# Performance work log

Measured on AMD Instinct MI355X. Metric: run time of the kernel, lower is better.

## Reference

```python
import jax, jax.numpy as jnp
import numpy as np

V = 50000      # tokenizer vocab size
E = 128        # embedding_dim
H = 160        # encoder_hidden_dim (bidirectional -> 2H)
D = 196        # decoder_hidden_dim
A = 224        # attention_dim
BN = 56        # bottle_neck_dim
PAD, START, END, UNK = 0, 1, 2, 3
COV_FACTOR = 0.75


def _lstm_step(x, h, c, Wi, Wh, bi, bh):
    # torch gate order: i, f, g, o
    g = x @ Wi.T + h @ Wh.T + bi + bh
    i, f, gg, o = jnp.split(g, 4, axis=-1)
    c = jax.nn.sigmoid(f) * c + jax.nn.sigmoid(i) * jnp.tanh(gg)
    h = jax.nn.sigmoid(o) * jnp.tanh(c)
    return h, c


def _run_lstm(x_tbe, Wi, Wh, bi, bh):
    B = x_tbe.shape[1]
    Hh = Wh.shape[1]
    def step(carry, xt):
        h, c = carry
        h, c = _lstm_step(xt, h, c, Wi, Wh, bi, bh)
        return (h, c), h
    init = (jnp.zeros((B, Hh), x_tbe.dtype), jnp.zeros((B, Hh), x_tbe.dtype))
    (hT, cT), hs = jax.lax.scan(step, init, x_tbe)
    return hs, hT, cT


def setup_inputs() -> dict:
    key = jax.random.key(0)
    ks = iter(jax.random.split(key, 48))
    def rn(shape, s=0.05):
        return jax.random.normal(next(ks), shape, jnp.float32) * s
    B, Tin, Ttgt = 32, 256, 100
    inp = {
        'batch_input_ids': jax.random.randint(next(ks), (B, Tin), 0, V + 50, dtype=jnp.int32),
        'batch_target_ids': jax.random.randint(next(ks), (B, Ttgt), 0, V + 50, dtype=jnp.int32),
        'max_num_oovs': 50,
        'emb': rn((V, E), 0.1),
        # bidirectional encoder LSTM
        'Wi_f': rn((4 * H, E)), 'Wh_f': rn((4 * H, H)),
        'bi_f': jnp.zeros(4 * H), 'bh_f': jnp.zeros(4 * H),
        'Wi_b': rn((4 * H, E)), 'Wh_b': rn((4 * H, H)),
        'bi_b': jnp.zeros(4 * H), 'bh_b': jnp.zeros(4 * H),
        # enc->dec bridges
        'Weh': rn((D, 2 * H)), 'beh': jnp.zeros(D),
        'Wec': rn((D, 2 * H)), 'bec': jnp.zeros(D),
        # decoder LSTMCell
        'Wi_d': rn((4 * D, E)), 'Wh_d': rn((4 * D, D)),
        'bi_d': jnp.zeros(4 * D), 'bh_d': jnp.zeros(4 * D),
        # attention
        'Wea': rn((A, 2 * H)), 'bea': jnp.zeros(A),
        'Wda': rn((A, D)),
        'Wca': rn((A, 1)),
        'v_attn': rn((1, A)),
        # vocab projection (bottleneck)
        'W1': rn((BN, D + 2 * H)), 'b1': jnp.zeros(BN),
        'W2': rn((V - END, BN)), 'b2': jnp.zeros(V - END),
        # p_gen switch
        'Wcs': rn((1, 2 * H)), 'bcs': jnp.zeros(1),
        'Wds': rn((1, D)),
        'Wes': rn((1, E)),
    }
    return inp


def reference(batch_input_ids, batch_target_ids, max_num_oovs, emb,
              Wi_f, Wh_f, bi_f, bh_f, Wi_b, Wh_b, bi_b, bh_b,
              Weh, beh, Wec, bec, Wi_d, Wh_d, bi_d, bh_d,
              Wea, bea, Wda, Wca, v_attn, W1, b1, W2, b2,
              Wcs, bcs, Wds, Wes):
    B, Tin = batch_input_ids.shape
    # map OOV input ids to <unk> for embedding lookup
    in_mapped = jnp.where(batch_input_ids >= V, UNK, batch_input_ids)
    x_tbe = emb[in_mapped].transpose(1, 0, 2)          # [Tin,B,E]
    hs_f, hTf, cTf = _run_lstm(x_tbe, Wi_f, Wh_f, bi_f, bh_f)
    hs_b, hTb, cTb = _run_lstm(x_tbe[::-1], Wi_b, Wh_b, bi_b, bh_b)
    enc = jnp.concatenate([hs_f, hs_b[::-1]], -1).transpose(1, 0, 2)  # [B,Tin,2H]
    h = jnp.concatenate([hTf, hTb], -1) @ Weh.T + beh   # [B,D]
    c = jnp.concatenate([cTf, cTb], -1) @ Wec.T + bec   # [B,D]
    enc_attn = enc @ Wea.T + bea                        # [B,Tin,A] (loop-invariant)
    pad_mask = batch_input_ids == PAD
    wca = Wca[:, 0]                                     # [A]
    cov0 = jnp.zeros((B, Tin))
    cur0 = jnp.full((B,), START, jnp.int32)

    def step(carry, nt):
        h, c, cov, cur, nll, cl = carry
        e = emb[cur]                                     # [B,E]
        h, c = _lstm_step(e, h, c, Wi_d, Wh_d, bi_d, bh_d)
        s = jnp.tanh(enc_attn + (h @ Wda.T)[:, None, :] + cov[:, :, None] * wca)
        s = s @ v_attn[0]                                # [B,Tin]
        s = jnp.where(pad_mask, -jnp.inf, s)
        attn = jax.nn.softmax(s, axis=1)                 # [B,Tin]
        ctx = jnp.einsum('bt,bth->bh', attn, enc)        # [B,2H]
        hc = jnp.concatenate([h, ctx], -1)
        vocab = jax.nn.softmax(jnp.tanh(hc @ W1.T + b1) @ W2.T + b2, axis=1)  # [B,V-END]
        p_gen = jax.nn.sigmoid(ctx @ Wcs[0] + bcs[0] + h @ Wds[0] + e @ Wes[0])  # [B]
        # F.pad(vocab, (END, max_num_oovs)).gather(1, nt): left-pad END zeros,
        # right-pad OOV zeros -> gen prob is vocab[nt-END] if END<=nt<V else 0
        idx = jnp.clip(nt - END, 0, vocab.shape[1] - 1)
        gen_p = jnp.take_along_axis(vocab, idx[:, None], axis=1)[:, 0]
        gen_p = jnp.where((nt >= END) & (nt < V), gen_p, 0.0)
        copy_p = jnp.sum(attn * (batch_input_ids == nt[:, None]), axis=1)
        p = p_gen * gen_p + (1.0 - p_gen) * copy_p
        nll = nll - jnp.log(p + 1e-9)
        cl = cl + jnp.minimum(attn, cov).sum(axis=1)
        cov = cov + attn
        cur = jnp.where(nt >= V, UNK, nt)
        return (h, c, cov, cur, nll, cl), None

    (h, c, cov, cur, nll, cl), _ = jax.lax.scan(
        step, (h, c, cov0, cur0, jnp.zeros(B), jnp.zeros(B)), batch_target_ids.T)
    nll_loss = nll.sum()
    cov_loss = cl.sum()
    return nll_loss, cov_loss, nll_loss + COV_FACTOR * cov_loss
```

## Files before the change

### kernel.cpp

```cpp
#include <hip/hip_runtime.h>

#define MSCOPE __HIP_MEMORY_SCOPE_AGENT


constexpr size_t oXf   = 0;
constexpr size_t oXb   = oXf   + (size_t)8192*640;
constexpr size_t oXd   = oXb   + (size_t)8192*640;
constexpr size_t oHencB= oXd   + (size_t)3200*784;
constexpr size_t oEncA = oHencB+ (size_t)64*256*160;
constexpr size_t oEs   = oEncA + (size_t)8192*224;
constexpr size_t oCT   = oEs   + 3200;
constexpr size_t oH0   = oCT   + 10240;
constexpr size_t oC0   = oH0   + 6272;
constexpr size_t oHWdsAll = oC0 + 6272;
constexpr size_t oCtxWAll = oHWdsAll + 3200;
constexpr size_t oCopyAll = oCtxWAll + 3200;
constexpr size_t oZidxAll = oCopyAll + 3200;
constexpr size_t oClAll   = oZidxAll + 3200;
constexpr size_t oNllWg   = oClAll + 32;
constexpr size_t oW1cT    = oNllWg + 192;
constexpr size_t oFEnd    = oW1cT + 17920;
constexpr size_t oHdAll   = 0;
constexpr size_t oUAll    = oHdAll + (size_t)100*6272;
constexpr size_t oUPreAll = oUAll  + (size_t)100*1792;
constexpr size_t oHwdaAll = oUPreAll + (size_t)100*1792;
constexpr size_t oPartAll = oHwdaAll + (size_t)100*7168;
#define FENC(d,t,p)  ((((d)*256 + (t))*20 + (p))*16)
#define FLSTM(s,p)   (163840 + ((s)*25 + (p))*16)
#define FAUX(s,p)    (203840 + ((s)*8 + (p))*16)
#define FP2(s,m,p)   (216640 + (((s)*4 + (m))*32 + (p))*16)
#define CP3          421440
#define CFIN         421456
constexpr int fEnd = 421472;

__device__ __forceinline__ float fast_tanh(float x){
  float e = __expf(-2.f*fabsf(x));
  float r = (1.f - e) * __builtin_amdgcn_rcpf(1.f + e);
  return copysignf(r, x);
}
__device__ __forceinline__ float sigm(float x){
  return __builtin_amdgcn_rcpf(1.f + __expf(-x));
}
__device__ __forceinline__ float aload(const float* p){
  return __hip_atomic_load(const_cast<float*>(p), __ATOMIC_RELAXED, MSCOPE);
}
__device__ __forceinline__ float2 aload2(const float* p){
  unsigned long long u = __hip_atomic_load(
      reinterpret_cast<unsigned long long*>(const_cast<float*>(p)),
      __ATOMIC_RELAXED, MSCOPE);
  float2 r; __builtin_memcpy(&r, &u, 8); return r;
}
__device__ __forceinline__ void astore(float* p, float v){
  __hip_atomic_store(p, v, __ATOMIC_RELAXED, MSCOPE);
}
__device__ __forceinline__ void set_line(unsigned* line){
  __hip_atomic_store(line, 1u, __ATOMIC_RELAXED, MSCOPE);
}
template<int SLP>
__device__ __forceinline__ void wait_lines(unsigned* base, int n, int tid){
  if (tid < 64){
    for(;;){
      bool miss = (tid < n) &&
        (__hip_atomic_load(base + tid*16, __ATOMIC_RELAXED, MSCOPE) == 0u);
      if (__ballot(miss) == 0ULL) break;
      __builtin_amdgcn_s_sleep(SLP);
    }
  }
  __syncthreads();
}
__device__ __forceinline__ void add1(unsigned* word){
  (void)__hip_atomic_fetch_add(word, 1u, __ATOMIC_RELAXED, MSCOPE);
}
__device__ __forceinline__ float block_sum(float v, float* red){
  #pragma unroll
  for (int o=32;o;o>>=1) v += __shfl_down(v,o);
  if ((threadIdx.x&63)==0) red[threadIdx.x>>6] = v;
  __syncthreads();
  v = red[0]+red[1]+red[2]+red[3];
  __syncthreads();
  return v;
}

__global__ void prep_kernel(const int* __restrict__ in_ids, const int* __restrict__ tgt,
                            int* __restrict__ in_mapped, int* __restrict__ cur_ids,
                            unsigned* __restrict__ flags){
  const int g0 = blockIdx.x*256 + threadIdx.x, stride = gridDim.x*256;
  for (int i = g0; i < 8192; i += stride){
    int t = i >> 5, b = i & 31;
    int id = in_ids[b*256 + t];
    in_mapped[i] = (id >= 50000) ? 3 : id;
  }
  for (int i = g0; i < 3200; i += stride){
    int k = i >> 5, b = i & 31;
    int id = (k == 0) ? 1 : tgt[b*100 + (k-1)];
    cur_ids[i] = (id >= 50000) ? 3 : id;
  }
  for (int i = g0; i < fEnd; i += stride) flags[i] = 0u;
}

__global__ void w1c_transpose(const float* __restrict__ W1, float* __restrict__ W1cT){
  int i = blockIdx.x*256 + threadIdx.x;
  if (i < 17920){ int q = i / 56, g = i - q*56; W1cT[q*56+g] = W1[(size_t)g*516 + 196 + q]; }
}

struct RGArgs{ const int* gid; const float* emb; const float* W;
               const float* bias1; const float* bias2; float* out; int N; };
__global__ void __launch_bounds__(256) rowgemm(RGArgs a){
  __shared__ float rl[8*128];
  const int tid = threadIdx.x;
  const int N = a.N;
  const size_t r0 = (size_t)blockIdx.x*8;
  const size_t t = r0 >> 5; const int b0 = (int)(r0 & 31);
  for (int i = tid; i < 8*128; i += 256){
    int r = i >> 7, k = i & 127;
    rl[i] = a.emb[(size_t)a.gid[r0+r]*128 + k];
  }
  __syncthreads();
  for (int g = tid; g < N; g += 256){
    const float* wr = a.W + (size_t)g*128;
    float acc[8];
    #pragma unroll
    for (int r=0;r<8;r++) acc[r]=0.f;
    for (int k=0;k<128;k+=4){
      float4 wv = *(const float4*)(wr+k);
      #pragma unroll
      for (int r=0;r<8;r++){
        float4 xv = *(const float4*)(rl + r*128 + k);
        acc[r] += wv.x*xv.x + wv.y*xv.y + wv.z*xv.z + wv.w*xv.w;
      }
    }
    float bias = a.bias1[g] + a.bias2[g];
    float* op = a.out + ((size_t)t*N + g)*32 + b0;
    *(float4*)(op)   = make_float4(acc[0]+bias,acc[1]+bias,acc[2]+bias,acc[3]+bias);
    *(float4*)(op+4) = make_float4(acc[4]+bias,acc[5]+bias,acc[6]+bias,acc[7]+bias);
  }
}

__global__ void es_kernel(const int* __restrict__ gid, const float* __restrict__ emb,
                          const float* __restrict__ Wes, float* __restrict__ es){
  int r = blockIdx.x, l = threadIdx.x;
  const float* e = emb + (size_t)gid[r]*128;
  float acc = e[l]*Wes[l] + e[l+64]*Wes[l+64];
  #pragma unroll
  for (int o=32;o;o>>=1) acc += __shfl_down(acc,o);
  if (l==0) es[r] = acc;
}

struct EncArgs{ const float* Xf; const float* Xb; const float* Whf; const float* Whb;
                float* hencB; float* cT; unsigned* flg; };
__global__ void __launch_bounds__(256) enc_scan(EncArgs a){
  extern __shared__ float sm[];
  float* Wl = sm;
  float* hl = sm + 5120;
  const int wg = blockIdx.x;
  const int dir = wg/20, jwg = wg%20;
// ... 57 lines not shown
  __shared__ float hc[320], cc[320];
  int b = blockIdx.x, tid = threadIdx.x;
  if (tid < 160){
    hc[tid]     = hencB[((size_t)b*256 + 255)*160 + tid];
    hc[160+tid] = hencB[((size_t)(32+b)*256 + 0)*160 + tid];
    cc[tid]     = cT[b*160 + tid];
    cc[160+tid] = cT[5120 + b*160 + tid];
  }
  __syncthreads();
  for (int g = tid; g < 196; g += 256){
    const float* w1 = Weh + (size_t)g*320;
    const float* w2 = Wec + (size_t)g*320;
    float a1 = beh[g], a2 = bec[g];
    for (int k = 0; k < 320; ++k){ a1 += hc[k]*w1[k]; a2 += cc[k]*w2[k]; }
    h0[b*196 + g] = a1;
    c0[b*196 + g] = a2;
  }
}

__global__ void __launch_bounds__(256) encA_gemm(const float* __restrict__ hencB,
                 const float* __restrict__ Wea, const float* __restrict__ bea,
                 float* __restrict__ encA){
  __shared__ float rl[8*320];
  const int tid = threadIdx.x;
  const size_t r0 = (size_t)blockIdx.x*8;
  for (int i = tid; i < 8*320; i += 256){
    int r = i/320, k = i - r*320;
    size_t row = r0 + r; int b = (int)(row >> 8), t = (int)(row & 255);
    rl[i] = (k < 160) ? hencB[((size_t)b*256 + t)*160 + k]
                      : hencB[((size_t)(32+b)*256 + t)*160 + (k-160)];
  }
  __syncthreads();
  for (int g = tid; g < 224; g += 256){
    const float* wr = Wea + (size_t)g*320;
    float acc[8];
    #pragma unroll
    for (int r=0;r<8;r++) acc[r]=0.f;
    for (int k=0;k<320;k+=4){
      float4 wv = *(const float4*)(wr+k);
      #pragma unroll
      for (int r=0;r<8;r++){
        float4 xv = *(const float4*)(rl + r*320 + k);
        acc[r] += wv.x*xv.x + wv.y*xv.y + wv.z*xv.z + wv.w*xv.w;
      }
    }
    float bias = bea[g];
    #pragma unroll
    for (int r=0;r<8;r++) encA[(r0+r)*224 + g] = acc[r] + bias;
  }
}

struct DecArgs{
  const float* Xd; const float* hencB; const float* encA;
  const float* h0; const float* c0;
  const float* Whd; const float* Wda; const float* Wca; const float* vat;
  const float* W1; const float* b1; const float* W1cT; const float* W2; const float* b2;
  const float* Wcs; const float* bcs; const float* Wds; const float* es;
  const int* in_ids; const int* tgt;
  float* hdAll; float* uAll; float* uPreAll; float* hwdaAll;
  float* hWdsAll; float* ctxWAll; float* copyAll;
  float* zidxAll; float* partAll; float* clAll; float* nllWg; float* out;
  unsigned* flg;
};

__device__ __forceinline__ void load_scr(const float* hp, float* scr, int tid){
  for (int i2 = tid; i2 < 3136; i2 += 256){
    float2 hv = aload2(hp + i2*2);
    int e = i2*2; int b2 = e & 31; int j2 = e >> 5;
    scr[b2*204 + j2]     = hv.x;
    scr[(b2+1)*204 + j2] = hv.y;
  }
}

__global__ void __launch_bounds__(256) dec_scan(DecArgs A){
  extern __shared__ float sm[];
  const int wg = blockIdx.x, tid = threadIdx.x;
  const int bp = tid & 31, jl = tid >> 5;
  unsigned* flg = A.flg;

  if (wg < 25){
    const int wl = wg;
    const int j = wl*8 + jl;
    float* Wl  = sm;
    float* scr = sm + 6272;
    for (int i = tid; i < 32*196; i += 256){
      int row = i/196, k = i - row*196;
      int gate = row >> 3, jj = row & 7;
      int jg = wl*8 + jj;
      Wl[i] = (jg < 196) ? A.Whd[((size_t)(gate*196 + jg))*196 + k] : 0.f;
    }
    float c = (j < 196) ? A.c0[bp*196 + j] : 0.f;
    for (int i = tid; i < 6272; i += 256){
      int bb = i/196, k = i - bb*196;
      scr[bb*204 + k] = A.h0[i];
    }
    const float4* w0 = (const float4*)(Wl + (0*8+jl)*196);
    const float4* w1 = (const float4*)(Wl + (1*8+jl)*196);
    const float4* w2 = (const float4*)(Wl + (2*8+jl)*196);
    const float4* w3 = (const float4*)(Wl + (3*8+jl)*196);
    __syncthreads();
    for (int s = 0; s < 100; ++s){
      float x0=0.f,x1=0.f,x2=0.f,x3=0.f;
      if (j < 196){
        const float* xr = A.Xd + ((size_t)s*784 + j)*32 + bp;
        x0 = xr[0]; x1 = xr[6272]; x2 = xr[12544]; x3 = xr[18816];
      }
      if (s > 0){
        wait_lines<2>(flg + FLSTM(s-1, 0), 25, tid);
        load_scr(A.hdAll + (size_t)(s-1)*6272, scr, tid);
      }
      __syncthreads();
      if (j < 196){
        float g0=x0,g1=x1,g2=x2,g3=x3;
        const float4* hr = (const float4*)(scr + bp*204);
        #pragma unroll 7
        for (int q = 0; q < 49; ++q){
          float4 hv = hr[q];
          float4 a0 = w0[q], a1 = w1[q], a2 = w2[q], a3 = w3[q];
          g0 += hv.x*a0.x + hv.y*a0.y + hv.z*a0.z + hv.w*a0.w;
          g1 += hv.x*a1.x + hv.y*a1.y + hv.z*a1.z + hv.w*a1.w;
          g2 += hv.x*a2.x + hv.y*a2.y + hv.z*a2.z + hv.w*a2.w;
          g3 += hv.x*a3.x + hv.y*a3.y + hv.z*a3.z + hv.w*a3.w;
        }
        float ig = sigm(g0), fg = sigm(g1), gc = fast_tanh(g2), og = sigm(g3);
        c = fg*c + ig*gc;
        float h = og * fast_tanh(c);
        astore(&A.hdAll[(size_t)s*6272 + j*32 + bp], h);
      }
      __syncthreads();
      if (tid == 0) set_line(flg + FLSTM(s, wl));
    }
    return;
  }

  if (wg < 33){
    const int a_ = wg - 25;
    float* wdaL = sm;
    float* w1hL = sm + 5488;
    float* WdsL = sm + 6860;
    float* scr  = sm + 7056;
    for (int i = tid; i < 28*196; i += 256){
      int al = i/196, k = i - al*196;
      wdaL[i] = A.Wda[(size_t)(a_*28 + al)*196 + k];
    }
    for (int i = tid; i < 7*196; i += 256){
      int gl = i/196, k = i - gl*196;
      w1hL[i] = A.W1[(size_t)(a_*7 + gl)*516 + k];
    }
    if (a_ == 7) for (int i = tid; i < 196; i += 256) WdsL[i] = A.Wds[i];
    __syncthreads();
    for (int s = 0; s < 100; ++s){
      wait_lines<2>(flg + FLSTM(s, 0), 25, tid);
      load_scr(A.hdAll + (size_t)s*6272, scr, tid);
      __syncthreads();
      for (int i = tid; i < 896; i += 256){
        int b2 = i & 31, al = i >> 5;
        const float4* h4 = (const float4*)(scr + b2*204);
        const float4* w4 = (const float4*)(wdaL + al*196);
        float acc = 0.f;
        #pragma unroll 7
        for (int q = 0; q < 49; ++q){
          float4 a4 = h4[q], b4 = w4[q];
          acc += a4.x*b4.x + a4.y*b4.y + a4.z*b4.z + a4.w*b4.w;
        }
        astore(&A.hwdaAll[(size_t)s*7168 + b2*224 + a_*28 + al], acc);
      }
      if (tid < 224){
        int b2 = tid & 31, gl = tid >> 5;
        int g = a_*7 + gl;
        const float4* h4 = (const float4*)(scr + b2*204);
        const float4* w4 = (const float4*)(w1hL + gl*196);
        float acc = A.b1[g];
        #pragma unroll 7
        for (int q = 0; q < 49; ++q){
          float4 a4 = h4[q], b4 = w4[q];
          acc += a4.x*b4.x + a4.y*b4.y + a4.z*b4.z + a4.w*b4.w;
        }
        astore(&A.uPreAll[(size_t)s*1792 + b2*56 + g], acc);
      }
      if (a_ == 7 && tid < 32){
        const float* hb = scr + tid*204;
        float acc = 0.f;
        #pragma unroll 4
        for (int q = 0; q < 196; ++q) acc += hb[q]*WdsL[q];
        astore(&A.hWdsAll[s*32 + tid], acc);
      }
      __syncthreads();
      if (tid == 0) set_line(flg + FAUX(s, a_));
    }
    return;
  }

  if (wg < 65){
    const int b = wg - 33;
    float* hwdaL = sm;
    float* attnL = sm + 224;
    float* pctx  = sm + 480;
    float* ctxL  = sm + 1440;
    float* red   = sm + 1760;
    float* pu    = sm + 1764;
    float* wcaL  = sm + 1988;
    float* vL    = sm + 2212;
    float* WcsL  = sm + 2436;
    if (tid < 224){ wcaL[tid] = A.Wca[tid]; vL[tid] = A.vat[tid]; }
    for (int i = tid; i < 320; i += 256) WcsL[i] = A.Wcs[i];
    const int inid = A.in_ids[b*256 + tid];
    const float4* erow = (const float4*)(A.encA + (size_t)(b*256 + tid)*224);
    float cov = 0.f, clr = 0.f;
    __syncthreads();
    for (int s = 0; s < 100; ++s){
      wait_lines<2>(flg + FAUX(s, 0), 8, tid);
      if (tid < 224) hwdaL[tid] = aload(&A.hwdaAll[(size_t)s*7168 + b*224 + tid]);
      __syncthreads();
      float exv = 0.f;
      if (inid != 0){
        float acc = 0.f;
        #pragma unroll 8
        for (int q = 0; q < 56; ++q){
          float4 ev = erow[q]; int a0 = 4*q;
          acc += fast_tanh(ev.x + hwdaL[a0]   + cov*wcaL[a0]  )*vL[a0];
          acc += fast_tanh(ev.y + hwdaL[a0+1] + cov*wcaL[a0+1])*vL[a0+1];
          acc += fast_tanh(ev.z + hwdaL[a0+2] + cov*wcaL[a0+2])*vL[a0+2];
          acc += fast_tanh(ev.w + hwdaL[a0+3] + cov*wcaL[a0+3])*vL[a0+3];
        }
        exv = __expf(acc);
      }
      float S = block_sum(exv, red);
      float attn = exv * __builtin_amdgcn_rcpf(S);
      attnL[tid] = attn;
      const int ntb = A.tgt[b*100 + s];
      float cpS = block_sum((inid == ntb) ? attn : 0.f, red);
      float mnS = block_sum(fminf(attn, cov), red);
      if (tid == 0){
        astore(&A.copyAll[s*32 + b], cpS);
        clr += mnS;
        if (s == 99) astore(&A.clAll[b], clr);
      }
      cov += attn;
      if (tid < 240){
        int seg = tid/80, h4i = tid - seg*80;
        int t0 = seg*86, t1 = (t0+86 < 256) ? t0+86 : 256;
        const float* base = (h4i < 40)
          ? (A.hencB + ((size_t)b*256)*160 + (size_t)h4i*4)
          : (A.hencB + ((size_t)(32+b)*256)*160 + (size_t)(h4i-40)*4);
        float4 accv = {0.f,0.f,0.f,0.f};
        #pragma unroll 4
        for (int t2 = t0; t2 < t1; ++t2){
          float av = attnL[t2];
          float4 ev = *(const float4*)(base + (size_t)t2*160);
          accv.x += av*ev.x; accv.y += av*ev.y; accv.z += av*ev.z; accv.w += av*ev.w;
        }
        *(float4*)(pctx + (seg*80+h4i)*4) = accv;
      }
      __syncthreads();
      if (tid < 80){
        float4 p0 = *(float4*)(pctx + tid*4);
        float4 p1 = *(float4*)(pctx + (80+tid)*4);
        float4 p2v = *(float4*)(pctx + (160+tid)*4);
        float4 cvv;
        cvv.x = p0.x+p1.x+p2v.x; cvv.y = p0.y+p1.y+p2v.y;
        cvv.z = p0.z+p1.z+p2v.z; cvv.w = p0.w+p1.w+p2v.w;
        *(float4*)(ctxL + tid*4) = cvv;
      }
      __syncthreads();
      if (tid < 224){
        int g = tid % 56, seg = tid / 56;
        float acc = 0.f;
        const float* wp = A.W1cT + (size_t)seg*80*56 + g;
        #pragma unroll 4
        for (int q = 0; q < 80; ++q) acc += ctxL[seg*80 + q] * wp[q*56];
        pu[seg*56 + g] = acc;
      } else {
        int l = tid - 224; float acc = 0.f;
        for (int q = l; q < 320; q += 32) acc += ctxL[q]*WcsL[q];
        #pragma unroll
        for (int o=16;o;o>>=1) acc += __shfl_down(acc,o,32);
        if (l==0) astore(&A.ctxWAll[s*32 + b], acc);
      }
      __syncthreads();
      if (tid < 56){
        float upre = aload(&A.uPreAll[(size_t)s*1792 + b*56 + tid]);
        float uu = fast_tanh(upre + pu[tid] + pu[56+tid] + pu[112+tid] + pu[168+tid]);
        astore(&A.uAll[(size_t)s*1792 + b*56 + tid], uu);
      }
      __syncthreads();
      if (tid == 0){
        set_line(flg + FP2(s,0,b));
        set_line(flg + FP2(s,1,b));
        set_line(flg + FP2(s,2,b));
        set_line(flg + FP2(s,3,b));
      }
    }
    return;
  }

  {
    const int wgv = wg - 65;
    const int vs = (int)(((long long)wgv*49998)/191);
    const int ve = (int)(((long long)(wgv+1)*49998)/191);
    const int r0v = vs + tid;
    const int r1v = vs + 256 + tid;
    const bool v1 = r1v < ve;
    float4 w2r0[14], w2r1[14];
    {
      const float4* wr = (const float4*)(A.W2 + (size_t)r0v*56);
      #pragma unroll
      for (int q=0;q<14;++q) w2r0[q] = wr[q];
      const float4* wr1 = (const float4*)(A.W2 + (size_t)(v1 ? r1v : vs)*56);
      #pragma unroll
      for (int q=0;q<14;++q) w2r1[q] = wr1[q];
    }
    const float b2v0 = A.b2[r0v];
    const float b2v1 = v1 ? A.b2[r1v] : 0.f;
    float* ulL  = sm;
    float* redW = sm + 1792;
    int*   idxL = (int*)(sm + 1920);
    float* red  = sm + 1952;
    const int lane = tid & 63, wv2 = tid >> 6;
    for (int s = 0; s < 100; ++s){
      int nt3 = (tid < 32) ? A.tgt[tid*100 + s] : 0;
      wait_lines<8>(flg + FP2(s, wgv & 3, 0), 32, tid);
      for (int i2 = tid; i2 < 896; i2 += 256){
        float2 u2 = aload2(&A.uAll[(size_t)s*1792 + i2*2]);
        *(float2*)(ulL + i2*2) = u2;
      }
      if (tid < 32){
        int ix = nt3 - 2; ix = ix<0?0:(ix>49997?49997:ix);
        idxL[tid] = ix;
      }
      __syncthreads();
      #pragma unroll 4
      for (int bb=0; bb<32; ++bb){
        const float4* uv = (const float4*)(ulL + bb*56);
        float z = b2v0;
        #pragma unroll
        for (int q=0;q<14;++q){
          float4 u4 = uv[q];
          z += w2r0[q].x*u4.x + w2r0[q].y*u4.y + w2r0[q].z*u4.z + w2r0[q].w*u4.w;
        }
        if (r0v == idxL[bb]) astore(&A.zidxAll[s*32+bb], z);
        float sv2 = __expf(z);
        if (v1){
          float z1 = b2v1;
          #pragma unroll
          for (int q=0;q<14;++q){
            float4 u4 = uv[q];
            z1 += w2r1[q].x*u4.x + w2r1[q].y*u4.y + w2r1[q].z*u4.z + w2r1[q].w*u4.w;
          }
          if (r1v == idxL[bb]) astore(&A.zidxAll[s*32+bb], z1);
          sv2 += __expf(z1);
        }
        #pragma unroll
        for (int o=32;o;o>>=1) sv2 += __shfl_down(sv2,o);
        if (lane == 0) redW[wv2*32+bb] = sv2;
      }
      __syncthreads();
      if (tid < 32){
        float tot = redW[tid]+redW[32+tid]+redW[64+tid]+redW[96+tid];
        astore(&A.partAll[(size_t)(s*32+tid)*191 + wgv], tot);
      }
      __syncthreads();
    }
    __syncthreads();
    if (tid == 0) add1(flg + CP3);
    if (tid == 0){
      while (__hip_atomic_load(flg + CP3, __ATOMIC_RELAXED, MSCOPE) != 191u)
        __builtin_amdgcn_s_sleep(32);
    }
    __syncthreads();
    float nll1 = 0.f;
    for (int p = wgv; p < 3200; p += 191){
      float pv = (tid < 191) ? aload(&A.partAll[(size_t)p*191 + tid]) : 0.f;
      float se = block_sum(pv, red);
      if (tid == 0){
        int s = p >> 5, b = p & 31;
        int nt2 = A.tgt[b*100 + s];
        float xg = aload(&A.ctxWAll[p]) + A.bcs[0] + aload(&A.hWdsAll[p]) + A.es[p];
        float pg = 1.f/(1.f + __expf(-xg));
        float genp = (nt2 >= 2 && nt2 < 50000) ? (__expf(aload(&A.zidxAll[p])) / se) : 0.f;
        float pr = pg*genp + (1.f-pg)*aload(&A.copyAll[p]);
        nll1 += -logf(pr + 1e-9f);
      }
    }
    if (tid == 0) astore(&A.nllWg[wgv], nll1);
    __syncthreads();
    if (tid == 0) add1(flg + CFIN);
    if (wg == 65){
      if (tid == 0){
        while (__hip_atomic_load(flg + CFIN, __ATOMIC_RELAXED, MSCOPE) != 191u)
          __builtin_amdgcn_s_sleep(32);
      }
      __syncthreads();
      float nv = (tid < 191) ? aload(&A.nllWg[tid]) : 0.f;
      float nll = block_sum(nv, red);
      float cv = (tid < 32) ? aload(&A.clAll[tid]) : 0.f;
      float cl = block_sum(cv, red);
      if (tid == 0){ A.out[0]=nll; A.out[1]=cl; A.out[2]=nll + 0.75f*cl; }
    }
  }
}

extern "C" void kernel_launch(void* const* d_in, const int* in_sizes, int n_in,
                              void* d_out, int out_size, void* d_ws, size_t ws_size,
                              hipStream_t stream){
  const int*   in_ids = (const int*)  d_in[0];
  const int*   tgt    = (const int*)  d_in[1];
  const float* emb    = (const float*)d_in[3];
  const float* Wi_f   = (const float*)d_in[4];
  const float* Wh_f   = (const float*)d_in[5];
  const float* bi_f   = (const float*)d_in[6];
  const float* bh_f   = (const float*)d_in[7];
  const float* Wi_b   = (const float*)d_in[8];
  const float* Wh_b   = (const float*)d_in[9];
  const float* bi_b   = (const float*)d_in[10];
  const float* bh_b   = (const float*)d_in[11];
  const float* Weh    = (const float*)d_in[12];
  const float* beh    = (const float*)d_in[13];
  const float* Wec    = (const float*)d_in[14];
  const float* bec    = (const float*)d_in[15];
  const float* Wi_d   = (const float*)d_in[16];
  const float* Wh_d   = (const float*)d_in[17];
  const float* bi_d   = (const float*)d_in[18];
  const float* bh_d   = (const float*)d_in[19];
  const float* Wea    = (const float*)d_in[20];
  const float* bea    = (const float*)d_in[21];
  const float* Wda    = (const float*)d_in[22];
  const float* Wca    = (const float*)d_in[23];
  const float* vat    = (const float*)d_in[24];
  const float* W1     = (const float*)d_in[25];
  const float* b1     = (const float*)d_in[26];
  const float* W2     = (const float*)d_in[27];
  const float* b2     = (const float*)d_in[28];
  const float* Wcs    = (const float*)d_in[29];
  const float* bcs    = (const float*)d_in[30];
  const float* Wds    = (const float*)d_in[31];
  const float* Wes    = (const float*)d_in[32];

  float* ws = (float*)d_ws;
  int* iBase = (int*)(ws + oFEnd);
  int* in_mapped = iBase;
  int* cur_ids   = iBase + 8192;
  unsigned* flags = (unsigned*)(iBase + 11392);

  prep_kernel<<<512, 256, 0, stream>>>(in_ids, tgt, in_mapped, cur_ids, flags);
  w1c_transpose<<<70, 256, 0, stream>>>(W1, ws + oW1cT);

  { RGArgs a{in_mapped, emb, Wi_f, bi_f, bh_f, ws + oXf, 640};
    rowgemm<<<1024, 256, 0, stream>>>(a); }
  { RGArgs a{in_mapped, emb, Wi_b, bi_b, bh_b, ws + oXb, 640};
    rowgemm<<<1024, 256, 0, stream>>>(a); }
  { RGArgs a{cur_ids, emb, Wi_d, bi_d, bh_d, ws + oXd, 784};
    rowgemm<<<400, 256, 0, stream>>>(a); }

  es_kernel<<<3200, 64, 0, stream>>>(cur_ids, emb, Wes, ws + oEs);

  { EncArgs ea{ws + oXf, ws + oXb, Wh_f, Wh_b, ws + oHencB, ws + oCT, flags};
    void* ka[] = {&ea};
    hipLaunchCooperativeKernel((void*)enc_scan, dim3(40), dim3(256), ka,
                               (unsigned)((5120 + 32*164)*4), stream); }

  mid_kernel<<<32, 256, 0, stream>>>(ws + oHencB, ws + oCT, Weh, beh, Wec, bec,
                                     ws + oH0, ws + oC0);

  encA_gemm<<<1024, 256, 0, stream>>>(ws + oHencB, Wea, bea, ws + oEncA);

  { DecArgs da{ws + oXd, ws + oHencB, ws + oEncA,
               ws + oH0, ws + oC0,
               Wh_d, Wda, Wca, vat,
               W1, b1, ws + oW1cT, W2, b2, Wcs, bcs, Wds, ws + oEs,
               in_ids, tgt,
               ws + oHdAll, ws + oUAll, ws + oUPreAll, ws + oHwdaAll,
               ws + oHWdsAll, ws + oCtxWAll, ws + oCopyAll,
               ws + oZidxAll, ws + oPartAll, ws + oClAll, ws + oNllWg, (float*)d_out,
               flags};
    void* ka[] = {&da};
    hipLaunchCooperativeKernel((void*)dec_scan, dim3(256), dim3(256), ka,
                               (unsigned)(13584*4), stream); }
}
```

Baseline: 4.925 ms.

## Add aggregator workgroup publishing watermark counters for cross-stage step flags

One workgroup (wg 65) is repurposed as a flag aggregator. It polls the per-step LSTM, aux and attention completion lines and publishes monotone watermark counters, replicated over 8 cache lines. Consumers now spin on a single watermark line with one thread instead of ballot-polling 8 to 32 lines each, and the attention stage sets one flag per batch instead of four copies. The intent is to cut polling traffic and contention on the flag lines. The cost is one fewer vocab workgroup (190 instead of 191) and an extra hop of latency through the aggregator.

```diff
diff --git a/kernel.cpp b/kernel.cpp
--- a/kernel.cpp
+++ b/kernel.cpp
@@ -28,10 +28,13 @@
 #define FENC(d,t,p)  ((((d)*256 + (t))*20 + (p))*16)
 #define FLSTM(s,p)   (163840 + ((s)*25 + (p))*16)
 #define FAUX(s,p)    (203840 + ((s)*8 + (p))*16)
-#define FP2(s,m,p)   (216640 + (((s)*4 + (m))*32 + (p))*16)
-#define CP3          421440
-#define CFIN         421456
-constexpr int fEnd = 421472;
+#define FP2(s,b)     (216640 + ((s)*32 + (b))*16)
+#define WML(r)       (267840 + (r)*16)
+#define WMA(r)       (267968 + (r)*16)
+#define WMP(r)       (268096 + (r)*16)
+#define CP3          268224
+#define CFIN         268240
+constexpr int fEnd = 268256;
 
 __device__ __forceinline__ float fast_tanh(float x){
   float e = __expf(-2.f*fabsf(x));
@@ -53,18 +56,30 @@
 __device__ __forceinline__ void astore(float* p, float v){
   __hip_atomic_store(p, v, __ATOMIC_RELAXED, MSCOPE);
 }
+__device__ __forceinline__ unsigned uload(unsigned* p){
+  return __hip_atomic_load(p, __ATOMIC_RELAXED, MSCOPE);
+}
 __device__ __forceinline__ void set_line(unsigned* line){
   __hip_atomic_store(line, 1u, __ATOMIC_RELAXED, MSCOPE);
+}
+__device__ __forceinline__ void ustore(unsigned* line, unsigned v){
+  __hip_atomic_store(line, v, __ATOMIC_RELAXED, MSCOPE);
 }
 template<int SLP>
 __device__ __forceinline__ void wait_lines(unsigned* base, int n, int tid){
   if (tid < 64){
     for(;;){
-      bool miss = (tid < n) &&
-        (__hip_atomic_load(base + tid*16, __ATOMIC_RELAXED, MSCOPE) == 0u);
+      bool miss = (tid < n) && (uload(base + tid*16) == 0u);
       if (__ballot(miss) == 0ULL) break;
       __builtin_amdgcn_s_sleep(SLP);
     }
+  }
+  __syncthreads();
+}
+template<int SLP>
+__device__ __forceinline__ void wait_wm(unsigned* line, unsigned target, int tid){
+  if (tid == 0){
+    while (uload(line) < target) __builtin_amdgcn_s_sleep(SLP);
   }
   __syncthreads();
 }
@@ -362,7 +377,7 @@
     if (a_ == 7) for (int i = tid; i < 196; i += 256) WdsL[i] = A.Wds[i];
     __syncthreads();
     for (int s = 0; s < 100; ++s){
-      wait_lines<2>(flg + FLSTM(s, 0), 25, tid);
+      wait_wm<2>(flg + WML(a_ & 7), (unsigned)(s+1), tid);
       load_scr(A.hdAll + (size_t)s*6272, scr, tid);
       __syncthreads();
       for (int i = tid; i < 896; i += 256){
@@ -421,7 +436,7 @@
     float cov = 0.f, clr = 0.f;
     __syncthreads();
     for (int s = 0; s < 100; ++s){
-      wait_lines<2>(flg + FAUX(s, 0), 8, tid);
+      wait_wm<2>(flg + WMA(b & 7), (unsigned)(s+1), tid);
       if (tid < 224) hwdaL[tid] = aload(&A.hwdaAll[(size_t)s*7168 + b*224 + tid]);
       __syncthreads();
       float exv = 0.f;
@@ -496,20 +511,50 @@
         astore(&A.uAll[(size_t)s*1792 + b*56 + tid], uu);
       }
       __syncthreads();
-      if (tid == 0){
-        set_line(flg + FP2(s,0,b));
-        set_line(flg + FP2(s,1,b));
-        set_line(flg + FP2(s,2,b));
-        set_line(flg + FP2(s,3,b));
-      }
+      if (tid == 0) set_line(flg + FP2(s, b));
     }
     return;
   }
 
+  if (wg == 65){
+    if (tid < 64){
+      int wmL = 0, wmA = 0, wmP = 0;
+      while (wmL < 100 || wmA < 100 || wmP < 100){
+        bool prog = false;
+        if (wmL < 100){
+          bool miss = (tid < 25) && (uload(flg + FLSTM(wmL, tid)) == 0u);
+          if (__ballot(miss) == 0ULL){
+            wmL++;
+            if (tid < 8) ustore(flg + WML(tid), (unsigned)wmL);
+            prog = true;
+          }
+        }
+        if (wmA < 100){
+          bool miss = (tid < 8) && (uload(flg + FAUX(wmA, tid)) == 0u);
+          if (__ballot(miss) == 0ULL){
+            wmA++;
+            if (tid < 8) ustore(flg + WMA(tid), (unsigned)wmA);
+            prog = true;
+          }
+        }
+        if (wmP < 100){
+          bool miss = (tid < 32) && (uload(flg + FP2(wmP, tid)) == 0u);
+          if (__ballot(miss) == 0ULL){
+            wmP++;
+            if (tid < 8) ustore(flg + WMP(tid), (unsigned)wmP);
+            prog = true;
+          }
+        }
+        if (!prog) __builtin_amdgcn_s_sleep(2);
+      }
+    }
+    return;
+  }
+
   {
-    const int wgv = wg - 65;
-    const int vs = (int)(((long long)wgv*49998)/191);
-    const int ve = (int)(((long long)(wgv+1)*49998)/191);
+    const int wgv = wg - 66;
+    const int vs = (int)(((long long)wgv*49998)/190);
+    const int ve = (int)(((long long)(wgv+1)*49998)/190);
     const int r0v = vs + tid;
     const int r1v = vs + 256 + tid;
     const bool v1 = r1v < ve;
@@ -531,7 +576,7 @@
     const int lane = tid & 63, wv2 = tid >> 6;
     for (int s = 0; s < 100; ++s){
       int nt3 = (tid < 32) ? A.tgt[tid*100 + s] : 0;
-      wait_lines<8>(flg + FP2(s, wgv & 3, 0), 32, tid);
+      wait_wm<8>(flg + WMP(wgv & 7), (unsigned)(s+1), tid);
       for (int i2 = tid; i2 < 896; i2 += 256){
         float2 u2 = aload2(&A.uAll[(size_t)s*1792 + i2*2]);
         *(float2*)(ulL + i2*2) = u2;
@@ -569,20 +614,19 @@
       __syncthreads();
       if (tid < 32){
         float tot = redW[tid]+redW[32+tid]+redW[64+tid]+redW[96+tid];
-        astore(&A.partAll[(size_t)(s*32+tid)*191 + wgv], tot);
+        astore(&A.partAll[(size_t)(s*32+tid)*190 + wgv], tot);
       }
       __syncthreads();
     }
     __syncthreads();
     if (tid == 0) add1(flg + CP3);
     if (tid == 0){
-      while (__hip_atomic_load(flg + CP3, __ATOMIC_RELAXED, MSCOPE) != 191u)
-        __builtin_amdgcn_s_sleep(32);
+      while (uload(flg + CP3) != 190u) __builtin_amdgcn_s_sleep(32);
     }
     __syncthreads();
     float nll1 = 0.f;
-    for (int p = wgv; p < 3200; p += 191){
-      float pv = (tid < 191) ? aload(&A.partAll[(size_t)p*191 + tid]) : 0.f;
+    for (int p = wgv; p < 3200; p += 190){
+      float pv = (tid < 190) ? aload(&A.partAll[(size_t)p*190 + tid]) : 0.f;
       float se = block_sum(pv, red);
       if (tid == 0){
         int s = p >> 5, b = p & 31;
@@ -597,13 +641,12 @@
     if (tid == 0) astore(&A.nllWg[wgv], nll1);
     __syncthreads();
     if (tid == 0) add1(flg + CFIN);
-    if (wg == 65){
+    if (wg == 66){
       if (tid == 0){
-        while (__hip_atomic_load(flg + CFIN, __ATOMIC_RELAXED, MSCOPE) != 191u)
-          __builtin_amdgcn_s_sleep(32);
-      }
-      __syncthreads();
-      float nv = (tid < 191) ? aload(&A.nllWg[tid]) : 0.f;
+        while (uload(flg + CFIN) != 190u) __builtin_amdgcn_s_sleep(32);
+      }
+      __syncthreads();
+      float nv = (tid < 190) ? aload(&A.nllWg[tid]) : 0.f;
       float nll = block_sum(nv, red);
       float cv = (tid < 32) ? aload(&A.clAll[tid]) : 0.f;
       float cl = block_sum(cv, red);
```

Result: no change. 4.936 ms (+0.2%).

## Run decoder LSTM recurrence in one workgroup with bf16 MFMA

Applied to the files above, without the earlier changes.

The decoder LSTM recurrence and the hidden-state projections (Wda, W1 hidden part, Wds) are merged into a single workgroup. That workgroup keeps h in LDS as bf16 fragments and computes gates with MFMA 16x16x32 bf16, using weights pre-packed by a new pack_af kernel. This removes the 25-workgroup cross-CU flag handshake and the global hdAll round trip on every step, and frees workgroups so the vocab softmax stage now spans 223 groups of one row per thread. The costs are bf16 rounding of the recurrent weights and state, a serial recurrence on one CU, and a switch from cooperative launch to a normal launch that relies on all workgroups being co-resident for the spin-waits.

```diff
diff --git a/kernel.cpp b/kernel.cpp
--- a/kernel.cpp
+++ b/kernel.cpp
@@ -1,6 +1,9 @@
 #include <hip/hip_runtime.h>
 
 #define MSCOPE __HIP_MEMORY_SCOPE_AGENT
+
+typedef __attribute__((ext_vector_type(8))) short bf16x8;
+typedef __attribute__((ext_vector_type(4))) float f32x4;
 
 
 constexpr size_t oXf   = 0;
@@ -18,20 +21,21 @@
 constexpr size_t oZidxAll = oCopyAll + 3200;
 constexpr size_t oClAll   = oZidxAll + 3200;
 constexpr size_t oNllWg   = oClAll + 32;
-constexpr size_t oW1cT    = oNllWg + 192;
-constexpr size_t oFEnd    = oW1cT + 17920;
-constexpr size_t oHdAll   = 0;
-constexpr size_t oUAll    = oHdAll + (size_t)100*6272;
+constexpr size_t oW1cT    = oNllWg + 224;
+constexpr size_t oAFl     = oW1cT + 17920;
+constexpr size_t oAFa     = oAFl + 93184;
+constexpr size_t oFEnd    = oAFa + 32256;
+constexpr size_t oUAll    = 0;
 constexpr size_t oUPreAll = oUAll  + (size_t)100*1792;
 constexpr size_t oHwdaAll = oUPreAll + (size_t)100*1792;
 constexpr size_t oPartAll = oHwdaAll + (size_t)100*7168;
 #define FENC(d,t,p)  ((((d)*256 + (t))*20 + (p))*16)
-#define FLSTM(s,p)   (163840 + ((s)*25 + (p))*16)
-#define FAUX(s,p)    (203840 + ((s)*8 + (p))*16)
-#define FP2(s,m,p)   (216640 + (((s)*4 + (m))*32 + (p))*16)
-#define CP3          421440
-#define CFIN         421456
-constexpr int fEnd = 421472;
+#define FL(s)        (163840 + (s)*16)
+#define FP2(s,m,b)   (165440 + (((s)*4 + (m))*32 + (b))*16)
+#define CP3          370240
+#define CFIN         370256
+constexpr int fEnd = 370272;
+constexpr unsigned ENC_FULL  = 0xFFFFFu;
 
 __device__ __forceinline__ float fast_tanh(float x){
   float e = __expf(-2.f*fabsf(x));
@@ -40,6 +44,10 @@
 }
 __device__ __forceinline__ float sigm(float x){
   return __builtin_amdgcn_rcpf(1.f + __expf(-x));
+}
+__device__ __forceinline__ unsigned bfr(float f){
+  unsigned u = __float_as_uint(f);
+  return (u + 0x7FFFu + ((u>>16)&1u)) >> 16;
 }
 __device__ __forceinline__ float aload(const float* p){
   return __hip_atomic_load(const_cast<float*>(p), __ATOMIC_RELAXED, MSCOPE);
@@ -53,6 +61,15 @@
 __device__ __forceinline__ void astore(float* p, float v){
   __hip_atomic_store(p, v, __ATOMIC_RELAXED, MSCOPE);
 }
+__device__ __forceinline__ void astore2(float* p, float a, float b){
+  float2 t; t.x = a; t.y = b;
+  unsigned long long u; __builtin_memcpy(&u, &t, 8);
+  __hip_atomic_store(reinterpret_cast<unsigned long long*>(p), u,
+                     __ATOMIC_RELAXED, MSCOPE);
+}
+__device__ __forceinline__ unsigned uload(unsigned* p){
+  return __hip_atomic_load(p, __ATOMIC_RELAXED, MSCOPE);
+}
 __device__ __forceinline__ void set_line(unsigned* line){
   __hip_atomic_store(line, 1u, __ATOMIC_RELAXED, MSCOPE);
 }
@@ -60,8 +77,7 @@
 __device__ __forceinline__ void wait_lines(unsigned* base, int n, int tid){
   if (tid < 64){
     for(;;){
-      bool miss = (tid < n) &&
-        (__hip_atomic_load(base + tid*16, __ATOMIC_RELAXED, MSCOPE) == 0u);
+      bool miss = (tid < n) && (uload(base + tid*16) == 0u);
       if (__ballot(miss) == 0ULL) break;
       __builtin_amdgcn_s_sleep(SLP);
     }
@@ -101,6 +117,48 @@
 __global__ void w1c_transpose(const float* __restrict__ W1, float* __restrict__ W1cT){
   int i = blockIdx.x*256 + threadIdx.x;
   if (i < 17920){ int q = i / 56, g = i - q*56; W1cT[q*56+g] = W1[(size_t)g*516 + 196 + q]; }
+}
+
+__global__ void pack_af(const float* __restrict__ Whd, float* __restrict__ AFl,
+                        const float* __restrict__ Wda, const float* __restrict__ W1,
+                        const float* __restrict__ Wds, float* __restrict__ AFa){
+  int dw = blockIdx.x*256 + threadIdx.x;
+  if (dw < 93184){
+    int frag = dw>>2, d = dw&3;
+    int T = frag/448, r2 = frag - T*448;
+    int k7 = r2>>6, l = r2&63;
+    int jb = T>>2, gate = T&3;
+    int j = jb*16 + (l&15);
+    int k0 = k7*32 + ((l>>4)<<3) + 2*d;
+    unsigned lo=0, hi=0;
+    if (j < 196){
+      if (k0   < 196) lo = bfr(Whd[(size_t)(gate*196+j)*196 + k0]);
+      if (k0+1 < 196) hi = bfr(Whd[(size_t)(gate*196+j)*196 + k0+1]);
+    }
+    ((unsigned*)AFl)[dw] = lo | (hi<<16);
+  }
+  if (dw < 32256){
+    int frag = dw>>2, d = dw&3;
+    int T = frag/448, r2 = frag - T*448;
+    int k7 = r2>>6, l = r2&63;
+    int ar = T*16 + (l&15);
+    int k0 = k7*32 + ((l>>4)<<3) + 2*d;
+    unsigned lo=0, hi=0;
+    #pragma unroll
+    for (int h = 0; h < 2; ++h){
+      int k = k0 + h;
+      float v = 0.f;
+      if (k < 196){
+        if (ar < 224) v = Wda[(size_t)ar*196 + k];
+        else { int g = ar - 224;
+          if (g < 56) v = W1[(size_t)g*516 + k];
+          else if (g == 56) v = Wds[k];
+        }
+      }
+      if (h == 0) lo = bfr(v); else hi = bfr(v);
+    }
+    ((unsigned*)AFa)[dw] = lo | (hi<<16);
+  }
 }
 
 struct RGArgs{ const int* gid; const float* emb; const float* W;
@@ -264,147 +322,163 @@
 
 struct DecArgs{
   const float* Xd; const float* hencB; const float* encA;
-  const float* h0; const float* c0;
-  const float* Whd; const float* Wda; const float* Wca; const float* vat;
-  const float* W1; const float* b1; const float* W1cT; const float* W2; const float* b2;
-  const float* Wcs; const float* bcs; const float* Wds; const float* es;
+  const float* h0; const float* c0; const float* AFl; const float* AFa;
+  const float* Wca; const float* vat; const float* W1cT; const float* b1;
+  const float* W2; const float* b2;
+  const float* Wcs; const float* bcs; const float* es;
   const int* in_ids; const int* tgt;
-  float* hdAll; float* uAll; float* uPreAll; float* hwdaAll;
+  float* uAll; float* uPreAll; float* hwdaAll;
   float* hWdsAll; float* ctxWAll; float* copyAll;
   float* zidxAll; float* partAll; float* clAll; float* nllWg; float* out;
   unsigned* flg;
 };
 
-__device__ __forceinline__ void load_scr(const float* hp, float* scr, int tid){
-  for (int i2 = tid; i2 < 3136; i2 += 256){
-    float2 hv = aload2(hp + i2*2);
-    int e = i2*2; int b2 = e & 31; int j2 = e >> 5;
-    scr[b2*204 + j2]     = hv.x;
-    scr[(b2+1)*204 + j2] = hv.y;
-  }
-}
-
 __global__ void __launch_bounds__(256) dec_scan(DecArgs A){
   extern __shared__ float sm[];
   const int wg = blockIdx.x, tid = threadIdx.x;
-  const int bp = tid & 31, jl = tid >> 5;
   unsigned* flg = A.flg;
 
-  if (wg < 25){
-    const int wl = wg;
-    const int j = wl*8 + jl;
-    float* Wl  = sm;
-    float* scr = sm + 6272;
-    for (int i = tid; i < 32*196; i += 256){
-      int row = i/196, k = i - row*196;
-      int gate = row >> 3, jj = row & 7;
-      int jg = wl*8 + jj;
-      Wl[i] = (jg < 196) ? A.Whd[((size_t)(gate*196 + jg))*196 + k] : 0.f;
-    }
-    float c = (j < 196) ? A.c0[bp*196 + j] : 0.f;
-    for (int i = tid; i < 6272; i += 256){
-      int bb = i/196, k = i - bb*196;
-      scr[bb*204 + k] = A.h0[i];
-    }
-    const float4* w0 = (const float4*)(Wl + (0*8+jl)*196);
-    const float4* w1 = (const float4*)(Wl + (1*8+jl)*196);
-    const float4* w2 = (const float4*)(Wl + (2*8+jl)*196);
-    const float4* w3 = (const float4*)(Wl + (3*8+jl)*196);
+  if (wg == 0){
+    unsigned* bfd = (unsigned*)sm;
+    bf16x8* bfp = (bf16x8*)sm;
+    const bf16x8* afl = (const bf16x8*)A.AFl;
+    const bf16x8* afa = (const bf16x8*)A.AFa;
+    const int l = tid & 63, wv = tid >> 6;
+    const int lq = l >> 4, lc = l & 15;
+    for (int dw = tid; dw < 3584; dw += 256){
+      int frag = dw>>2, d = dw&3;
+      int knt = frag>>6, fl2 = frag&63;
+      int nt = knt&1, k7 = knt>>1;
+      int j0 = k7*32 + ((fl2>>4)<<3) + 2*d;
+      int b = nt*16 + (fl2&15);
+      unsigned lo = (j0   < 196) ? bfr(A.h0[b*196 + j0])   : 0u;
+      unsigned hi = (j0+1 < 196) ? bfr(A.h0[b*196 + j0+1]) : 0u;
+      bfd[dw] = lo | (hi<<16);
+    }
+    float cst[4][2][4];
+    #pragma unroll
+    for (int n = 0; n < 4; ++n){
+      int jb = wv + 4*n;
+      #pragma unroll
+      for (int nt = 0; nt < 2; ++nt){
+        int b = nt*16 + lc;
+        #pragma unroll
+        for (int i = 0; i < 4; ++i){
+          int j = jb*16 + lq*4 + i;
+          cst[n][nt][i] = (jb < 13 && j < 196) ? A.c0[b*196 + j] : 0.f;
+        }
+      }
+    }
     __syncthreads();
+    bf16x8 Bfr[7][2];
+    #pragma unroll
+    for (int k7 = 0; k7 < 7; ++k7)
+      #pragma unroll
+      for (int nt = 0; nt < 2; ++nt)
+        Bfr[k7][nt] = bfp[(k7*2+nt)*64 + l];
+
+    float hreg[4][2][4];
     for (int s = 0; s < 100; ++s){
-      float x0=0.f,x1=0.f,x2=0.f,x3=0.f;
-      if (j < 196){
-        const float* xr = A.Xd + ((size_t)s*784 + j)*32 + bp;
-        x0 = xr[0]; x1 = xr[6272]; x2 = xr[12544]; x3 = xr[18816];
-      }
-      if (s > 0){
-        wait_lines<2>(flg + FLSTM(s-1, 0), 25, tid);
-        load_scr(A.hdAll + (size_t)(s-1)*6272, scr, tid);
-      }
-      __syncthreads();
-      if (j < 196){
-        float g0=x0,g1=x1,g2=x2,g3=x3;
-        const float4* hr = (const float4*)(scr + bp*204);
-        #pragma unroll 7
-        for (int q = 0; q < 49; ++q){
-          float4 hv = hr[q];
-          float4 a0 = w0[q], a1 = w1[q], a2 = w2[q], a3 = w3[q];
-          g0 += hv.x*a0.x + hv.y*a0.y + hv.z*a0.z + hv.w*a0.w;
-          g1 += hv.x*a1.x + hv.y*a1.y + hv.z*a1.z + hv.w*a1.w;
-          g2 += hv.x*a2.x + hv.y*a2.y + hv.z*a2.z + hv.w*a2.w;
-          g3 += hv.x*a3.x + hv.y*a3.y + hv.z*a3.z + hv.w*a3.w;
+      const float* Xs = A.Xd + (size_t)s*25088;
+      #pragma unroll
+      for (int n = 0; n < 4; ++n){
+        int jb = wv + 4*n;
+        if (jb < 13){
+          f32x4 acc[2][4];
+          #pragma unroll
+          for (int g = 0; g < 4; ++g){
+            int T = jb*4 + g;
+            const bf16x8* afT = afl + (size_t)T*7*64 + l;
+            f32x4 a0 = {0.f,0.f,0.f,0.f}, a1 = {0.f,0.f,0.f,0.f};
+            #pragma unroll
+            for (int k7 = 0; k7 < 7; ++k7){
+              bf16x8 af = afT[k7*64];
+              a0 = __builtin_amdgcn_mfma_f32_16x16x32_bf16(af, Bfr[k7][0], a0, 0,0,0);
+              a1 = __builtin_amdgcn_mfma_f32_16x16x32_bf16(af, Bfr[k7][1], a1, 0,0,0);
+            }
+            acc[0][g] = a0; acc[1][g] = a1;
+          }
+          #pragma unroll
+          for (int nt = 0; nt < 2; ++nt){
+            int b = nt*16 + lc;
+            #pragma unroll
+            for (int i = 0; i < 4; ++i){
+              int j = jb*16 + lq*4 + i;
+              float xi=0.f, xf=0.f, xg=0.f, xo=0.f;
+              if (j < 196){
+                xi = Xs[((size_t)(0*196+j))*32 + b];
+                xf = Xs[((size_t)(196+j))*32 + b];
+                xg = Xs[((size_t)(392+j))*32 + b];
+                xo = Xs[((size_t)(588+j))*32 + b];
+              }
+              float I = acc[nt][0][i] + xi, F = acc[nt][1][i] + xf;
+              float G = acc[nt][2][i] + xg, O = acc[nt][3][i] + xo;
+              float cc = sigm(F)*cst[n][nt][i] + sigm(I)*fast_tanh(G);
+              cst[n][nt][i] = cc;
+              hreg[n][nt][i] = sigm(O)*fast_tanh(cc);
+            }
+          }
         }
-        float ig = sigm(g0), fg = sigm(g1), gc = fast_tanh(g2), og = sigm(g3);
-        c = fg*c + ig*gc;
-        float h = og * fast_tanh(c);
-        astore(&A.hdAll[(size_t)s*6272 + j*32 + bp], h);
-      }
-      __syncthreads();
-      if (tid == 0) set_line(flg + FLSTM(s, wl));
+      }
+      __syncthreads();
+      #pragma unroll
+      for (int n = 0; n < 4; ++n){
+        int jb = wv + 4*n;
+        if (jb < 13){
+          #pragma unroll
+          for (int nt = 0; nt < 2; ++nt){
+            #pragma unroll
+            for (int p = 0; p < 2; ++p){
+              int jp = jb*16 + lq*4 + 2*p;
+              if (jp < 196){
+                int k7 = jp>>5, tl = lc | (((jp>>3)&3)<<4), d = (jp&7)>>1;
+                bfd[((k7*2+nt)*64 + tl)*4 + d] =
+                  bfr(hreg[n][nt][2*p]) | (bfr(hreg[n][nt][2*p+1])<<16);
+              }
+            }
+          }
+        }
+      }
+      __syncthreads();
+      #pragma unroll
+      for (int k7 = 0; k7 < 7; ++k7)
+        #pragma unroll
+        for (int nt = 0; nt < 2; ++nt)
+          Bfr[k7][nt] = bfp[(k7*2+nt)*64 + l];
+      for (int m = 0; m < 5; ++m){
+        int T = wv + 4*m;
+        if (T < 18){
+          const bf16x8* afT = afa + (size_t)T*7*64 + l;
+          #pragma unroll
+          for (int nt = 0; nt < 2; ++nt){
+            f32x4 acc = {0.f,0.f,0.f,0.f};
+            #pragma unroll
+            for (int k7 = 0; k7 < 7; ++k7)
+              acc = __builtin_amdgcn_mfma_f32_16x16x32_bf16(afT[k7*64], Bfr[k7][nt], acc, 0,0,0);
+            int b = nt*16 + lc;
+            #pragma unroll
+            for (int p = 0; p < 2; ++p){
+              int ar = T*16 + lq*4 + 2*p;
+              float v0 = acc[2*p], v1 = acc[2*p+1];
+              if (ar < 224){
+                astore2(&A.hwdaAll[(size_t)s*7168 + b*224 + ar], v0, v1);
+              } else {
+                int g = ar - 224;
+                if (g < 56) astore2(&A.uPreAll[(size_t)s*1792 + b*56 + g], v0, v1);
+                else if (g == 56) astore(&A.hWdsAll[s*32 + b], v0);
+              }
+            }
+          }
+        }
+      }
+      __syncthreads();
+      if (tid == 0) set_line(flg + FL(s));
     }
     return;
   }
 
   if (wg < 33){
-    const int a_ = wg - 25;
-    float* wdaL = sm;
-    float* w1hL = sm + 5488;
-    float* WdsL = sm + 6860;
-    float* scr  = sm + 7056;
-    for (int i = tid; i < 28*196; i += 256){
-      int al = i/196, k = i - al*196;
-      wdaL[i] = A.Wda[(size_t)(a_*28 + al)*196 + k];
-    }
-    for (int i = tid; i < 7*196; i += 256){
-      int gl = i/196, k = i - gl*196;
-      w1hL[i] = A.W1[(size_t)(a_*7 + gl)*516 + k];
-    }
-    if (a_ == 7) for (int i = tid; i < 196; i += 256) WdsL[i] = A.Wds[i];
-    __syncthreads();
-    for (int s = 0; s < 100; ++s){
-      wait_lines<2>(flg + FLSTM(s, 0), 25, tid);
-      load_scr(A.hdAll + (size_t)s*6272, scr, tid);
-      __syncthreads();
-      for (int i = tid; i < 896; i += 256){
-        int b2 = i & 31, al = i >> 5;
-        const float4* h4 = (const float4*)(scr + b2*204);
-        const float4* w4 = (const float4*)(wdaL + al*196);
-        float acc = 0.f;
-        #pragma unroll 7
-        for (int q = 0; q < 49; ++q){
-          float4 a4 = h4[q], b4 = w4[q];
-          acc += a4.x*b4.x + a4.y*b4.y + a4.z*b4.z + a4.w*b4.w;
-        }
-        astore(&A.hwdaAll[(size_t)s*7168 + b2*224 + a_*28 + al], acc);
-      }
-      if (tid < 224){
-        int b2 = tid & 31, gl = tid >> 5;
-        int g = a_*7 + gl;
-        const float4* h4 = (const float4*)(scr + b2*204);
-        const float4* w4 = (const float4*)(w1hL + gl*196);
-        float acc = A.b1[g];
-        #pragma unroll 7
-        for (int q = 0; q < 49; ++q){
-          float4 a4 = h4[q], b4 = w4[q];
-          acc += a4.x*b4.x + a4.y*b4.y + a4.z*b4.z + a4.w*b4.w;
-        }
-        astore(&A.uPreAll[(size_t)s*1792 + b2*56 + g], acc);
-      }
-      if (a_ == 7 && tid < 32){
-        const float* hb = scr + tid*204;
-        float acc = 0.f;
-        #pragma unroll 4
-        for (int q = 0; q < 196; ++q) acc += hb[q]*WdsL[q];
-        astore(&A.hWdsAll[s*32 + tid], acc);
-      }
-      __syncthreads();
-      if (tid == 0) set_line(flg + FAUX(s, a_));
-    }
-    return;
-  }
-
-  if (wg < 65){
-    const int b = wg - 33;
+    const int b = wg - 1;
     float* hwdaL = sm;
     float* attnL = sm + 224;
     float* pctx  = sm + 480;
@@ -414,14 +488,16 @@
     float* wcaL  = sm + 1988;
     float* vL    = sm + 2212;
     float* WcsL  = sm + 2436;
+    float* b1L   = sm + 2756;
     if (tid < 224){ wcaL[tid] = A.Wca[tid]; vL[tid] = A.vat[tid]; }
     for (int i = tid; i < 320; i += 256) WcsL[i] = A.Wcs[i];
+    if (tid < 56) b1L[tid] = A.b1[tid];
     const int inid = A.in_ids[b*256 + tid];
     const float4* erow = (const float4*)(A.encA + (size_t)(b*256 + tid)*224);
     float cov = 0.f, clr = 0.f;
     __syncthreads();
     for (int s = 0; s < 100; ++s){
-      wait_lines<2>(flg + FAUX(s, 0), 8, tid);
+      wait_lines<2>(flg + FL(s), 1, tid);
       if (tid < 224) hwdaL[tid] = aload(&A.hwdaAll[(size_t)s*7168 + b*224 + tid]);
       __syncthreads();
       float exv = 0.f;
@@ -492,7 +568,7 @@
       __syncthreads();
       if (tid < 56){
         float upre = aload(&A.uPreAll[(size_t)s*1792 + b*56 + tid]);
-        float uu = fast_tanh(upre + pu[tid] + pu[56+tid] + pu[112+tid] + pu[168+tid]);
+        float uu = fast_tanh(upre + b1L[tid] + pu[tid] + pu[56+tid] + pu[112+tid] + pu[168+tid]);
         astore(&A.uAll[(size_t)s*1792 + b*56 + tid], uu);
       }
       __syncthreads();
@@ -507,23 +583,19 @@
   }
 
   {
-    const int wgv = wg - 65;
-    const int vs = (int)(((long long)wgv*49998)/191);
-    const int ve = (int)(((long long)(wgv+1)*49998)/191);
-    const int r0v = vs + tid;
-    const int r1v = vs + 256 + tid;
-    const bool v1 = r1v < ve;
-    float4 w2r0[14], w2r1[14];
+    const int wgv = wg - 33;
+    const int vs = (int)(((long long)wgv*49998)/223);
+    const int ve = (int)(((long long)(wgv+1)*49998)/223);
+    const int v = vs + tid;
+    const bool valid = v < ve;
+    const int vc = valid ? v : 0;
+    float4 w2r[14];
     {
-      const float4* wr = (const float4*)(A.W2 + (size_t)r0v*56);
+      const float4* wr = (const float4*)(A.W2 + (size_t)vc*56);
       #pragma unroll
-      for (int q=0;q<14;++q) w2r0[q] = wr[q];
-      const float4* wr1 = (const float4*)(A.W2 + (size_t)(v1 ? r1v : vs)*56);
-      #pragma unroll
-      for (int q=0;q<14;++q) w2r1[q] = wr1[q];
-    }
-    const float b2v0 = A.b2[r0v];
-    const float b2v1 = v1 ? A.b2[r1v] : 0.f;
+      for (int q=0;q<14;++q) w2r[q] = wr[q];
+    }
+    const float b2v = A.b2[vc];
     float* ulL  = sm;
     float* redW = sm + 1792;
     int*   idxL = (int*)(sm + 1920);
@@ -544,24 +616,14 @@
       #pragma unroll 4
       for (int bb=0; bb<32; ++bb){
         const float4* uv = (const float4*)(ulL + bb*56);
-        float z = b2v0;
+        float z = b2v;
         #pragma unroll
         for (int q=0;q<14;++q){
           float4 u4 = uv[q];
-          z += w2r0[q].x*u4.x + w2r0[q].y*u4.y + w2r0[q].z*u4.z + w2r0[q].w*u4.w;
+          z += w2r[q].x*u4.x + w2r[q].y*u4.y + w2r[q].z*u4.z + w2r[q].w*u4.w;
         }
-        if (r0v == idxL[bb]) astore(&A.zidxAll[s*32+bb], z);
-        float sv2 = __expf(z);
-        if (v1){
-          float z1 = b2v1;
-          #pragma unroll
-          for (int q=0;q<14;++q){
-            float4 u4 = uv[q];
-            z1 += w2r1[q].x*u4.x + w2r1[q].y*u4.y + w2r1[q].z*u4.z + w2r1[q].w*u4.w;
-          }
-          if (r1v == idxL[bb]) astore(&A.zidxAll[s*32+bb], z1);
-          sv2 += __expf(z1);
-        }
+        if (valid && v == idxL[bb]) astore(&A.zidxAll[s*32+bb], z);
+        float sv2 = valid ? __expf(z) : 0.f;
         #pragma unroll
         for (int o=32;o;o>>=1) sv2 += __shfl_down(sv2,o);
         if (lane == 0) redW[wv2*32+bb] = sv2;
@@ -569,20 +631,19 @@
       __syncthreads();
       if (tid < 32){
         float tot = redW[tid]+redW[32+tid]+redW[64+tid]+redW[96+tid];
-        astore(&A.partAll[(size_t)(s*32+tid)*191 + wgv], tot);
+        astore(&A.partAll[(size_t)(s*32+tid)*223 + wgv], tot);
       }
       __syncthreads();
     }
     __syncthreads();
     if (tid == 0) add1(flg + CP3);
     if (tid == 0){
-      while (__hip_atomic_load(flg + CP3, __ATOMIC_RELAXED, MSCOPE) != 191u)
-        __builtin_amdgcn_s_sleep(32);
+      while (uload(flg + CP3) != 223u) __builtin_amdgcn_s_sleep(32);
     }
     __syncthreads();
     float nll1 = 0.f;
-    for (int p = wgv; p < 3200; p += 191){
-      float pv = (tid < 191) ? aload(&A.partAll[(size_t)p*191 + tid]) : 0.f;
+    for (int p = wgv; p < 3200; p += 223){
+      float pv = (tid < 223) ? aload(&A.partAll[(size_t)p*223 + tid]) : 0.f;
       float se = block_sum(pv, red);
       if (tid == 0){
         int s = p >> 5, b = p & 31;
@@ -597,13 +658,12 @@
     if (tid == 0) astore(&A.nllWg[wgv], nll1);
     __syncthreads();
     if (tid == 0) add1(flg + CFIN);
-    if (wg == 65){
+    if (wg == 33){
       if (tid == 0){
-        while (__hip_atomic_load(flg + CFIN, __ATOMIC_RELAXED, MSCOPE) != 191u)
-          __builtin_amdgcn_s_sleep(32);
-      }
-      __syncthreads();
-      float nv = (tid < 191) ? aload(&A.nllWg[tid]) : 0.f;
+        while (uload(flg + CFIN) != 223u) __builtin_amdgcn_s_sleep(32);
+      }
+      __syncthreads();
+      float nv = (tid < 223) ? aload(&A.nllWg[tid]) : 0.f;
       float nll = block_sum(nv, red);
       float cv = (tid < 32) ? aload(&A.clAll[tid]) : 0.f;
       float cl = block_sum(cv, red);
@@ -656,6 +716,7 @@
 
   prep_kernel<<<512, 256, 0, stream>>>(in_ids, tgt, in_mapped, cur_ids, flags);
   w1c_transpose<<<70, 256, 0, stream>>>(W1, ws + oW1cT);
+  pack_af<<<364, 256, 0, stream>>>(Wh_d, ws + oAFl, Wda, W1, Wds, ws + oAFa);
 
   { RGArgs a{in_mapped, emb, Wi_f, bi_f, bh_f, ws + oXf, 640};
     rowgemm<<<1024, 256, 0, stream>>>(a); }
@@ -677,15 +738,12 @@
   encA_gemm<<<1024, 256, 0, stream>>>(ws + oHencB, Wea, bea, ws + oEncA);
 
   { DecArgs da{ws + oXd, ws + oHencB, ws + oEncA,
-               ws + oH0, ws + oC0,
-               Wh_d, Wda, Wca, vat,
-               W1, b1, ws + oW1cT, W2, b2, Wcs, bcs, Wds, ws + oEs,
+               ws + oH0, ws + oC0, ws + oAFl, ws + oAFa,
+               Wca, vat, ws + oW1cT, b1, W2, b2, Wcs, bcs, ws + oEs,
                in_ids, tgt,
-               ws + oHdAll, ws + oUAll, ws + oUPreAll, ws + oHwdaAll,
+               ws + oUAll, ws + oUPreAll, ws + oHwdaAll,
                ws + oHWdsAll, ws + oCtxWAll, ws + oCopyAll,
                ws + oZidxAll, ws + oPartAll, ws + oClAll, ws + oNllWg, (float*)d_out,
                flags};
-    void* ka[] = {&da};
-    hipLaunchCooperativeKernel((void*)dec_scan, dim3(256), dim3(256), ka,
-                               (unsigned)(13584*4), stream); }
-}
+    dec_scan<<<dim3(256), dim3(256), 3584*4, stream>>>(da); }
+}
```

Result: slower. 6.588 ms (+33.8%).
